# Optimization experiments

Measured on AMD Instinct MI355X. Metric: run time of the kernel, lower is better.

The kernel has to match this reference:

```python
import jax, jax.numpy as jnp
import numpy as np


def setup_inputs() -> dict:
    key = jax.random.key(0)
    ks = jax.random.split(key, 6)
    B, N, S, D, A = 32, 12, 512, 256, 96
    return {
        "value": jax.random.normal(ks[0], (B, N, S, D), dtype=jnp.float32),
        "emb": jax.random.normal(ks[1], (N, S, A), dtype=jnp.float32),
        "Wqk": jax.random.normal(ks[2], (A, D), dtype=jnp.float32) * (A ** -0.5),
        "bqk": jax.random.normal(ks[3], (D,), dtype=jnp.float32) * 0.02,
        "Wv": jax.random.normal(ks[4], (D, D), dtype=jnp.float32) * (D ** -0.5),
        "bv": jax.random.normal(ks[5], (D,), dtype=jnp.float32) * 0.02,
    }


def reference(value, emb, Wqk, bqk, Wv, bv):
    # qk: [n, s, d] -- query and key share the same projection FC_Q_K
    qk = emb @ Wqk + bqk
    v = value @ Wv + bv                      # [b, n, s, d]
    q = jax.nn.softmax(qk, axis=-1)          # softmax over d (last dim of query)
    k = jax.nn.softmax(qk.swapaxes(-1, -2), axis=-1)  # [n, d, s], softmax over s
    # key @ value: [n, d, s] x [b, n, s, e] -> [b, n, d, e] (broadcast over b)
    kv = jnp.einsum('nds,bnse->bnde', k, v)
    # query @ kv: [n, s, d] x [b, n, d, e] -> [b, n, s, e]
    out = jnp.einsum('nsd,bnde->bnse', q, kv)
    return out
```

## Files before the change

### kernel.cpp

```cpp
#include <hip/hip_runtime.h>
#include <hip/hip_bf16.h>

#define B_ 32
#define N_ 12
#define S_ 512
#define D_ 256
#define A_ 96

typedef __attribute__((ext_vector_type(8))) short short8;
typedef __attribute__((ext_vector_type(4))) float float4v;

static __device__ __forceinline__ ushort f2bf(float f) {
  union { float f; unsigned u; } a;
  a.f = f;
  return (ushort)((a.u + 0x7FFFu + ((a.u >> 16) & 1u)) >> 16);
}

__global__ __launch_bounds__(256) void k_qk_softmax_q(
    const float* __restrict__ emb, const float* __restrict__ Wqk,
    const float* __restrict__ bqk, float* __restrict__ qk,
    ushort* __restrict__ qb) {
  int ns = blockIdx.x;
  int d = threadIdx.x;
  __shared__ float se[A_];
  __shared__ float red[8];
  if (d < A_) se[d] = emb[ns * A_ + d];
  __syncthreads();
  float acc = bqk[d];
#pragma unroll
  for (int a = 0; a < A_; ++a) acc = fmaf(se[a], Wqk[a * D_ + d], acc);
  qk[ns * D_ + d] = acc;
  float m = acc;
  for (int off = 32; off; off >>= 1) m = fmaxf(m, __shfl_xor(m, off));
  if ((d & 63) == 0) red[d >> 6] = m;
  __syncthreads();
  m = fmaxf(fmaxf(red[0], red[1]), fmaxf(red[2], red[3]));
  float e = __expf(acc - m);
  float sum = e;
  for (int off = 32; off; off >>= 1) sum += __shfl_xor(sum, off);
  if ((d & 63) == 0) red[4 + (d >> 6)] = sum;
  __syncthreads();
  sum = red[4] + red[5] + red[6] + red[7];
  qb[ns * D_ + d] = f2bf(e / sum);
}

__global__ __launch_bounds__(256) void k_softmax_kT(
    const float* __restrict__ qk, ushort* __restrict__ kTb) {
  int d = blockIdx.x;
  int n = blockIdx.y;
  int s = threadIdx.x;
  __shared__ float red[8];
  float v0 = qk[(n * S_ + s) * D_ + d];
  float v1 = qk[(n * S_ + s + 256) * D_ + d];
  float m = fmaxf(v0, v1);
  for (int off = 32; off; off >>= 1) m = fmaxf(m, __shfl_xor(m, off));
  if ((s & 63) == 0) red[s >> 6] = m;
  __syncthreads();
  m = fmaxf(fmaxf(red[0], red[1]), fmaxf(red[2], red[3]));
  float e0 = __expf(v0 - m), e1 = __expf(v1 - m);
  float sum = e0 + e1;
  for (int off = 32; off; off >>= 1) sum += __shfl_xor(sum, off);
  if ((s & 63) == 0) red[4 + (s >> 6)] = sum;
  __syncthreads();
  sum = red[4] + red[5] + red[6] + red[7];
  float inv = 1.0f / sum;
  kTb[(n * D_ + d) * S_ + s] = f2bf(e0 * inv);
  kTb[(n * D_ + d) * S_ + s + 256] = f2bf(e1 * inv);
}

__global__ __launch_bounds__(256) void k_wvt(const float* __restrict__ Wv,
                                             ushort* __restrict__ WvT) {
  int c = blockIdx.x, e = threadIdx.x;
  WvT[c * D_ + e] = f2bf(Wv[e * D_ + c]);
}

__global__ __launch_bounds__(256) void k_kv0T(
    const ushort* __restrict__ kTb, const float* __restrict__ value,
    ushort* __restrict__ kv0T) {
  const int bx = blockIdx.x;
  const int by = blockIdx.y;
  const int bz = blockIdx.z;
  const int n = bz % N_;
  const int tid = threadIdx.x;
  const int l = tid & 63, w = tid >> 6;
  const int wm = w & 1, wn = w >> 1;
  const int lane16 = l & 15, quad = l >> 4;

  __shared__ ushort ldsA[128 * 72];
  __shared__ ushort ldsB[128 * 72];

  float4v acc[4][4];
#pragma unroll
  for (int i = 0; i < 4; ++i)
#pragma unroll
    for (int j = 0; j < 4; ++j) acc[i][j] = (float4v)0.0f;

  const ushort* kTbase = kTb + ((size_t)(n * D_ + bx * 128)) * S_;
  const float* vbase = value + (size_t)bz * S_ * D_ + by * 128;

  for (int sc = 0; sc < S_; sc += 64) {
    __syncthreads();
#pragma unroll
    for (int it = 0; it < 4; ++it) {
      int id = it * 256 + tid;
      int rd = id >> 3, cc = (id & 7) * 8;
      *(uint4*)(&ldsA[rd * 72 + cc]) =
          *(const uint4*)(kTbase + rd * S_ + sc + cc);
    }
#pragma unroll
    for (int it = 0; it < 16; ++it) {
      int id = it * 256 + tid;
      int e = id & 127, sp = id >> 7;
      float f0 = vbase[(sc + 2 * sp) * D_ + e];
      float f1 = vbase[(sc + 2 * sp + 1) * D_ + e];
      ushort2 p;
      p.x = f2bf(f0);
      p.y = f2bf(f1);
      *(ushort2*)(&ldsB[e * 72 + 2 * sp]) = p;
    }
    __syncthreads();
#pragma unroll
    for (int kc = 0; kc < 64; kc += 32) {
      int ko = kc + quad * 8;
      short8 a[4], b[4];
#pragma unroll
      for (int i = 0; i < 4; ++i)
        a[i] = *(const short8*)(&ldsA[(wm * 64 + i * 16 + lane16) * 72 + ko]);
#pragma unroll
      for (int j = 0; j < 4; ++j)
        b[j] = *(const short8*)(&ldsB[(wn * 64 + j * 16 + lane16) * 72 + ko]);
#pragma unroll
      for (int i = 0; i < 4; ++i)
#pragma unroll
        for (int j = 0; j < 4; ++j)
          acc[i][j] = __builtin_amdgcn_mfma_f32_16x16x32_bf16(a[i], b[j],
                                                              acc[i][j], 0, 0, 0);
    }
  }
  ushort* obase = kv0T + (size_t)bz * D_ * D_;
#pragma unroll
  for (int i = 0; i < 4; ++i) {
#pragma unroll
    for (int j = 0; j < 4; ++j) {
      int e = by * 128 + wn * 64 + j * 16 + lane16;
      int d0 = bx * 128 + wm * 64 + i * 16 + quad * 4;
      ushort4 p;
      p.x = f2bf(acc[i][j][0]);
      p.y = f2bf(acc[i][j][1]);
      p.z = f2bf(acc[i][j][2]);
      p.w = f2bf(acc[i][j][3]);
      *(ushort4*)(obase + e * D_ + d0) = p;
    }
  }
}

__global__ __launch_bounds__(256) void k_out_fused(
    const ushort* __restrict__ qb, const ushort* __restrict__ kv0T,
    const ushort* __restrict__ WvT, const float* __restrict__ bv,
    float* __restrict__ out) {
  const int bx = blockIdx.x;
  const int bz = blockIdx.y;
  const int n = bz % N_;
  const int tid = threadIdx.x;
  const int l = tid & 63, w = tid >> 6;
  const int lane16 = l & 15, quad = l >> 4;

  __shared__ ushort smem[35328];
  ushort* ldsKV = smem;
  ushort* ldsQ = smem + 18432;
  ushort* ldsW = smem;
  ushort* ldsT = smem + 18432;

  const ushort* qbase = qb + ((size_t)n * S_ + bx * 64) * D_;
  const ushort* kvbase = kv0T + (size_t)bz * D_ * D_;

  float4v acc[4][4];
#pragma unroll
  for (int i = 0; i < 4; ++i)
#pragma unroll
    for (int j = 0; j < 4; ++j) acc[i][j] = (float4v)0.0f;

  for (int dc = 0; dc < D_; dc += 64) {
    __syncthreads();
#pragma unroll
    for (int it = 0; it < 2; ++it) {
      int id = it * 256 + tid;
      int r = id >> 3, cc = (id & 7) * 8;
      *(uint4*)(&ldsQ[r * 72 + cc]) = *(const uint4*)(qbase + r * D_ + dc + cc);
    }
#pragma unroll
    for (int it = 0; it < 8; ++it) {
      int id = it * 256 + tid;
      int r = id >> 3, cc = (id & 7) * 8;
      *(uint4*)(&ldsKV[r * 72 + cc]) =
          *(const uint4*)(kvbase + r * D_ + dc + cc);
    }
    __syncthreads();
#pragma unroll
    for (int kc = 0; kc < 64; kc += 32) {
      int ko = kc + quad * 8;
      short8 a[4], b[4];
#pragma unroll
      for (int i = 0; i < 4; ++i)
        a[i] = *(const short8*)(&ldsKV[(w * 64 + i * 16 + lane16) * 72 + ko]);
#pragma unroll
      for (int j = 0; j < 4; ++j)
        b[j] = *(const short8*)(&ldsQ[(j * 16 + lane16) * 72 + ko]);
#pragma unroll
      for (int i = 0; i < 4; ++i)
#pragma unroll
        for (int j = 0; j < 4; ++j)
          acc[i][j] = __builtin_amdgcn_mfma_f32_16x16x32_bf16(a[i], b[j],
                                                              acc[i][j], 0, 0, 0);
    }
  }
  __syncthreads();
#pragma unroll
  for (int i = 0; i < 4; ++i) {
#pragma unroll
    for (int j = 0; j < 4; ++j) {
      int s = j * 16 + lane16;
      int e0 = w * 64 + i * 16 + quad * 4;
      ushort4 p;
      p.x = f2bf(acc[i][j][0]);
      p.y = f2bf(acc[i][j][1]);
      p.z = f2bf(acc[i][j][2]);
      p.w = f2bf(acc[i][j][3]);
      *(ushort4*)(&ldsT[s * 264 + e0]) = p;
    }
  }

  float4v acc2[4][4];
#pragma unroll
  for (int i = 0; i < 4; ++i)
#pragma unroll
    for (int j = 0; j < 4; ++j) acc2[i][j] = (float4v)0.0f;

  for (int ec = 0; ec < D_; ec += 64) {
    __syncthreads();
#pragma unroll
    for (int it = 0; it < 8; ++it) {
      int id = it * 256 + tid;
      int r = id >> 3, cc = (id & 7) * 8;
      *(uint4*)(&ldsW[r * 72 + cc]) = *(const uint4*)(WvT + r * D_ + ec + cc);
    }
    __syncthreads();
#pragma unroll
    for (int kc = 0; kc < 64; kc += 32) {
      int ko = kc + quad * 8;
      short8 a[4], b[4];
#pragma unroll
      for (int i = 0; i < 4; ++i)
        a[i] = *(const short8*)(&ldsT[(i * 16 + lane16) * 264 + ec + ko]);
#pragma unroll
      for (int j = 0; j < 4; ++j)
        b[j] = *(const short8*)(&ldsW[(w * 64 + j * 16 + lane16) * 72 + ko]);
#pragma unroll
      for (int i = 0; i < 4; ++i)
#pragma unroll
        for (int j = 0; j < 4; ++j)
          acc2[i][j] = __builtin_amdgcn_mfma_f32_16x16x32_bf16(a[i], b[j],
                                                               acc2[i][j], 0, 0, 0);
    }
  }
  float* obase = out + (size_t)bz * S_ * D_ + (size_t)bx * 64 * D_;
#pragma unroll
  for (int i = 0; i < 4; ++i) {
#pragma unroll
    for (int j = 0; j < 4; ++j) {
      int s0 = i * 16 + quad * 4;
      int c = w * 64 + j * 16 + lane16;
      float bvc = bv[c];
#pragma unroll
      for (int r = 0; r < 4; ++r)
        obase[(s0 + r) * D_ + c] = acc2[i][j][r] + bvc;
    }
  }
}

extern "C" void kernel_launch(void* const* d_in, const int* in_sizes, int n_in,
                              void* d_out, int out_size, void* d_ws,
                              size_t ws_size, hipStream_t stream) {
  const float* value = (const float*)d_in[0];
  const float* emb   = (const float*)d_in[1];
  const float* Wqk   = (const float*)d_in[2];
  const float* bqk   = (const float*)d_in[3];
  const float* Wv    = (const float*)d_in[4];
  const float* bv    = (const float*)d_in[5];
  float* out = (float*)d_out;

  char* ws = (char*)d_ws;
  float*  qk   = (float*)ws;
  ushort* qb   = (ushort*)(ws + 6291456);
  ushort* kTb  = (ushort*)(ws + 9437184);
  ushort* kv0T = (ushort*)(ws + 12582912);
  ushort* WvT  = (ushort*)(ws + 62914560);

  k_qk_softmax_q<<<dim3(N_ * S_), 256, 0, stream>>>(emb, Wqk, bqk, qk, qb);
  k_softmax_kT<<<dim3(D_, N_), 256, 0, stream>>>(qk, kTb);
  k_wvt<<<dim3(D_), 256, 0, stream>>>(Wv, WvT);
  k_kv0T<<<dim3(2, 2, B_ * N_), 256, 0, stream>>>(kTb, value, kv0T);
  k_out_fused<<<dim3(8, B_ * N_), 256, 0, stream>>>(qb, kv0T, WvT, bv, out);
}
```

Baseline: 483.7 us.

## Reassociate Wv into kv and split into three direct-to-LDS bf16 GEMMs

Adds a separate pass that transposes value and converts it to bf16. The per-(b,n) chain is then computed as three generic 128x128 GEMM kernels: kv0 = kT·v, then kv0 is multiplied by Wv (the reassociation, a 256x256x256 product), then q times that result plus bias. All three share a core that loads tiles with global_load_lds instead of register-staged copies. This removes the fused two-stage output kernel and its per-block Wv recompute, at the cost of an extra full transposed copy of value and more intermediate buffers written to and read from HBM. The unpadded 64-wide LDS rows may cause bank conflicts.

```diff
diff --git a/kernel.cpp b/kernel.cpp
--- a/kernel.cpp
+++ b/kernel.cpp
@@ -9,6 +9,13 @@
 
 typedef __attribute__((ext_vector_type(8))) short short8;
 typedef __attribute__((ext_vector_type(4))) float float4v;
+
+typedef const __attribute__((address_space(1))) void* gas_cvp;
+typedef __attribute__((address_space(3))) void* las_vp;
+
+static __device__ __forceinline__ void gl_lds16(const ushort* g, ushort* l) {
+  __builtin_amdgcn_global_load_lds((gas_cvp)g, (las_vp)l, 16, 0, 0);
+}
 
 static __device__ __forceinline__ ushort f2bf(float f) {
   union { float f; unsigned u; } a;
@@ -74,207 +81,152 @@
   WvT[c * D_ + e] = f2bf(Wv[e * D_ + c]);
 }
 
-__global__ __launch_bounds__(256) void k_kv0T(
-    const ushort* __restrict__ kTb, const float* __restrict__ value,
-    ushort* __restrict__ kv0T) {
-  const int bx = blockIdx.x;
-  const int by = blockIdx.y;
-  const int bz = blockIdx.z;
-  const int n = bz % N_;
+__global__ __launch_bounds__(256) void k_vT(const float* __restrict__ value,
+                                            ushort* __restrict__ vTb) {
+  const int s0 = blockIdx.x * 64;
+  const int e0 = blockIdx.y * 64;
+  const size_t bz = blockIdx.z;
+  __shared__ ushort lds[64 * 72];
+  const float* vb = value + bz * (size_t)(S_ * D_);
+  const int tid = threadIdx.x;
+#pragma unroll
+  for (int t = 0; t < 4; ++t) {
+    int id = t * 256 + tid;
+    int r = id >> 4;
+    int c4 = id & 15;
+    float4 f = *(const float4*)(vb + (size_t)(s0 + r) * D_ + e0 + c4 * 4);
+    lds[(c4 * 4 + 0) * 72 + r] = f2bf(f.x);
+    lds[(c4 * 4 + 1) * 72 + r] = f2bf(f.y);
+    lds[(c4 * 4 + 2) * 72 + r] = f2bf(f.z);
+    lds[(c4 * 4 + 3) * 72 + r] = f2bf(f.w);
+  }
+  __syncthreads();
+  ushort* ob = vTb + bz * (size_t)(D_ * S_);
+#pragma unroll
+  for (int t = 0; t < 2; ++t) {
+    int id = t * 256 + tid;
+    int e = id >> 3;
+    int c8 = id & 7;
+    *(uint4*)(ob + (size_t)(e0 + e) * S_ + s0 + c8 * 8) =
+        *(const uint4*)(&lds[e * 72 + c8 * 8]);
+  }
+}
+
+static __device__ __forceinline__ void gemm_core_128(
+    const ushort* __restrict__ A, const ushort* __restrict__ B, int lda,
+    int ldb, int K, ushort* ldsA, ushort* ldsB, float4v acc[4][4]) {
   const int tid = threadIdx.x;
   const int l = tid & 63, w = tid >> 6;
-  const int wm = w & 1, wn = w >> 1;
-  const int lane16 = l & 15, quad = l >> 4;
-
-  __shared__ ushort ldsA[128 * 72];
-  __shared__ ushort ldsB[128 * 72];
-
-  float4v acc[4][4];
+  const int lane16 = l & 15, quad = l >> 4;
+  const int wm = w & 1, wn = w >> 1;
+  const int lrow = l >> 3;
+  const int lcol = (l & 7) * 8;
 #pragma unroll
   for (int i = 0; i < 4; ++i)
 #pragma unroll
     for (int j = 0; j < 4; ++j) acc[i][j] = (float4v)0.0f;
-
-  const ushort* kTbase = kTb + ((size_t)(n * D_ + bx * 128)) * S_;
-  const float* vbase = value + (size_t)bz * S_ * D_ + by * 128;
-
-  for (int sc = 0; sc < S_; sc += 64) {
+  for (int kc = 0; kc < K; kc += 64) {
     __syncthreads();
 #pragma unroll
-    for (int it = 0; it < 4; ++it) {
-      int id = it * 256 + tid;
-      int rd = id >> 3, cc = (id & 7) * 8;
-      *(uint4*)(&ldsA[rd * 72 + cc]) =
-          *(const uint4*)(kTbase + rd * S_ + sc + cc);
-    }
-#pragma unroll
-    for (int it = 0; it < 16; ++it) {
-      int id = it * 256 + tid;
-      int e = id & 127, sp = id >> 7;
-      float f0 = vbase[(sc + 2 * sp) * D_ + e];
-      float f1 = vbase[(sc + 2 * sp + 1) * D_ + e];
-      ushort2 p;
-      p.x = f2bf(f0);
-      p.y = f2bf(f1);
-      *(ushort2*)(&ldsB[e * 72 + 2 * sp]) = p;
+    for (int t = 0; t < 4; ++t) {
+      int row = w * 32 + t * 8;
+      gl_lds16(A + (size_t)(row + lrow) * lda + kc + lcol,
+               &ldsA[row * 64]);
+      gl_lds16(B + (size_t)(row + lrow) * ldb + kc + lcol,
+               &ldsB[row * 64]);
     }
     __syncthreads();
 #pragma unroll
-    for (int kc = 0; kc < 64; kc += 32) {
-      int ko = kc + quad * 8;
+    for (int kk = 0; kk < 64; kk += 32) {
+      const int ko = kk + quad * 8;
       short8 a[4], b[4];
 #pragma unroll
       for (int i = 0; i < 4; ++i)
-        a[i] = *(const short8*)(&ldsA[(wm * 64 + i * 16 + lane16) * 72 + ko]);
+        a[i] = *(const short8*)&ldsA[(wm * 64 + i * 16 + lane16) * 64 + ko];
 #pragma unroll
       for (int j = 0; j < 4; ++j)
-        b[j] = *(const short8*)(&ldsB[(wn * 64 + j * 16 + lane16) * 72 + ko]);
+        b[j] = *(const short8*)&ldsB[(wn * 64 + j * 16 + lane16) * 64 + ko];
 #pragma unroll
       for (int i = 0; i < 4; ++i)
 #pragma unroll
         for (int j = 0; j < 4; ++j)
-          acc[i][j] = __builtin_amdgcn_mfma_f32_16x16x32_bf16(a[i], b[j],
-                                                              acc[i][j], 0, 0, 0);
+          acc[i][j] = __builtin_amdgcn_mfma_f32_16x16x32_bf16(
+              a[i], b[j], acc[i][j], 0, 0, 0);
     }
   }
-  ushort* obase = kv0T + (size_t)bz * D_ * D_;
-#pragma unroll
-  for (int i = 0; i < 4; ++i) {
-#pragma unroll
-    for (int j = 0; j < 4; ++j) {
-      int e = by * 128 + wn * 64 + j * 16 + lane16;
-      int d0 = bx * 128 + wm * 64 + i * 16 + quad * 4;
-      ushort4 p;
-      p.x = f2bf(acc[i][j][0]);
-      p.y = f2bf(acc[i][j][1]);
-      p.z = f2bf(acc[i][j][2]);
-      p.w = f2bf(acc[i][j][3]);
-      *(ushort4*)(obase + e * D_ + d0) = p;
-    }
-  }
-}
-
-__global__ __launch_bounds__(256) void k_out_fused(
-    const ushort* __restrict__ qb, const ushort* __restrict__ kv0T,
-    const ushort* __restrict__ WvT, const float* __restrict__ bv,
-    float* __restrict__ out) {
-  const int bx = blockIdx.x;
-  const int bz = blockIdx.y;
+}
+
+__global__ __launch_bounds__(256) void k_gemm1(
+    const ushort* __restrict__ kTb, const ushort* __restrict__ vTb,
+    ushort* __restrict__ kv0) {
+  __shared__ ushort ldsA[128 * 64], ldsB[128 * 64];
+  const int bx = blockIdx.x, by = blockIdx.y, bz = blockIdx.z;
   const int n = bz % N_;
-  const int tid = threadIdx.x;
-  const int l = tid & 63, w = tid >> 6;
-  const int lane16 = l & 15, quad = l >> 4;
-
-  __shared__ ushort smem[35328];
-  ushort* ldsKV = smem;
-  ushort* ldsQ = smem + 18432;
-  ushort* ldsW = smem;
-  ushort* ldsT = smem + 18432;
-
-  const ushort* qbase = qb + ((size_t)n * S_ + bx * 64) * D_;
-  const ushort* kvbase = kv0T + (size_t)bz * D_ * D_;
-
   float4v acc[4][4];
+  gemm_core_128(kTb + ((size_t)n * D_ + bx * 128) * S_,
+                vTb + ((size_t)bz * D_ + by * 128) * S_, S_, S_, S_, ldsA,
+                ldsB, acc);
+  const int l = threadIdx.x & 63, w = threadIdx.x >> 6;
+  const int lane16 = l & 15, quad = l >> 4;
+  const int wm = w & 1, wn = w >> 1;
+  ushort* C = kv0 + (size_t)bz * D_ * D_;
 #pragma unroll
   for (int i = 0; i < 4; ++i)
 #pragma unroll
-    for (int j = 0; j < 4; ++j) acc[i][j] = (float4v)0.0f;
-
-  for (int dc = 0; dc < D_; dc += 64) {
-    __syncthreads();
-#pragma unroll
-    for (int it = 0; it < 2; ++it) {
-      int id = it * 256 + tid;
-      int r = id >> 3, cc = (id & 7) * 8;
-      *(uint4*)(&ldsQ[r * 72 + cc]) = *(const uint4*)(qbase + r * D_ + dc + cc);
-    }
-#pragma unroll
-    for (int it = 0; it < 8; ++it) {
-      int id = it * 256 + tid;
-      int r = id >> 3, cc = (id & 7) * 8;
-      *(uint4*)(&ldsKV[r * 72 + cc]) =
-          *(const uint4*)(kvbase + r * D_ + dc + cc);
-    }
-    __syncthreads();
-#pragma unroll
-    for (int kc = 0; kc < 64; kc += 32) {
-      int ko = kc + quad * 8;
-      short8 a[4], b[4];
-#pragma unroll
-      for (int i = 0; i < 4; ++i)
-        a[i] = *(const short8*)(&ldsKV[(w * 64 + i * 16 + lane16) * 72 + ko]);
-#pragma unroll
-      for (int j = 0; j < 4; ++j)
-        b[j] = *(const short8*)(&ldsQ[(j * 16 + lane16) * 72 + ko]);
-#pragma unroll
-      for (int i = 0; i < 4; ++i)
-#pragma unroll
-        for (int j = 0; j < 4; ++j)
-          acc[i][j] = __builtin_amdgcn_mfma_f32_16x16x32_bf16(a[i], b[j],
-                                                              acc[i][j], 0, 0, 0);
-    }
-  }
-  __syncthreads();
-#pragma unroll
-  for (int i = 0; i < 4; ++i) {
-#pragma unroll
-    for (int j = 0; j < 4; ++j) {
-      int s = j * 16 + lane16;
-      int e0 = w * 64 + i * 16 + quad * 4;
-      ushort4 p;
-      p.x = f2bf(acc[i][j][0]);
-      p.y = f2bf(acc[i][j][1]);
-      p.z = f2bf(acc[i][j][2]);
-      p.w = f2bf(acc[i][j][3]);
-      *(ushort4*)(&ldsT[s * 264 + e0]) = p;
-    }
-  }
-
-  float4v acc2[4][4];
+    for (int j = 0; j < 4; ++j)
+#pragma unroll
+      for (int r = 0; r < 4; ++r)
+        C[(size_t)(bx * 128 + wm * 64 + i * 16 + quad * 4 + r) * D_ +
+          by * 128 + wn * 64 + j * 16 + lane16] = f2bf(acc[i][j][r]);
+}
+
+__global__ __launch_bounds__(256) void k_gemm2(
+    const ushort* __restrict__ WvT, const ushort* __restrict__ kv0,
+    ushort* __restrict__ kvWT) {
+  __shared__ ushort ldsA[128 * 64], ldsB[128 * 64];
+  const int bx = blockIdx.x, by = blockIdx.y, bz = blockIdx.z;
+  float4v acc[4][4];
+  gemm_core_128(WvT + (size_t)(bx * 128) * D_,
+                kv0 + (size_t)bz * D_ * D_ + (size_t)(by * 128) * D_, D_, D_,
+                D_, ldsA, ldsB, acc);
+  const int l = threadIdx.x & 63, w = threadIdx.x >> 6;
+  const int lane16 = l & 15, quad = l >> 4;
+  const int wm = w & 1, wn = w >> 1;
+  ushort* C = kvWT + (size_t)bz * D_ * D_;
 #pragma unroll
   for (int i = 0; i < 4; ++i)
 #pragma unroll
-    for (int j = 0; j < 4; ++j) acc2[i][j] = (float4v)0.0f;
-
-  for (int ec = 0; ec < D_; ec += 64) {
-    __syncthreads();
-#pragma unroll
-    for (int it = 0; it < 8; ++it) {
-      int id = it * 256 + tid;
-      int r = id >> 3, cc = (id & 7) * 8;
-      *(uint4*)(&ldsW[r * 72 + cc]) = *(const uint4*)(WvT + r * D_ + ec + cc);
-    }
-    __syncthreads();
-#pragma unroll
-    for (int kc = 0; kc < 64; kc += 32) {
-      int ko = kc + quad * 8;
-      short8 a[4], b[4];
-#pragma unroll
-      for (int i = 0; i < 4; ++i)
-        a[i] = *(const short8*)(&ldsT[(i * 16 + lane16) * 264 + ec + ko]);
-#pragma unroll
-      for (int j = 0; j < 4; ++j)
-        b[j] = *(const short8*)(&ldsW[(w * 64 + j * 16 + lane16) * 72 + ko]);
-#pragma unroll
-      for (int i = 0; i < 4; ++i)
-#pragma unroll
-        for (int j = 0; j < 4; ++j)
-          acc2[i][j] = __builtin_amdgcn_mfma_f32_16x16x32_bf16(a[i], b[j],
-                                                               acc2[i][j], 0, 0, 0);
-    }
-  }
-  float* obase = out + (size_t)bz * S_ * D_ + (size_t)bx * 64 * D_;
-#pragma unroll
-  for (int i = 0; i < 4; ++i) {
-#pragma unroll
-    for (int j = 0; j < 4; ++j) {
-      int s0 = i * 16 + quad * 4;
-      int c = w * 64 + j * 16 + lane16;
-      float bvc = bv[c];
+    for (int j = 0; j < 4; ++j)
 #pragma unroll
       for (int r = 0; r < 4; ++r)
-        obase[(s0 + r) * D_ + c] = acc2[i][j][r] + bvc;
-    }
+        C[(size_t)(bx * 128 + wm * 64 + i * 16 + quad * 4 + r) * D_ +
+          by * 128 + wn * 64 + j * 16 + lane16] = f2bf(acc[i][j][r]);
+}
+
+__global__ __launch_bounds__(256) void k_gemm3(
+    const ushort* __restrict__ qb, const ushort* __restrict__ kvWT,
+    const float* __restrict__ bv, float* __restrict__ out) {
+  __shared__ ushort ldsA[128 * 64], ldsB[128 * 64];
+  const int bx = blockIdx.x, by = blockIdx.y, bz = blockIdx.z;
+  const int n = bz % N_;
+  float4v acc[4][4];
+  gemm_core_128(qb + ((size_t)n * S_ + bx * 128) * D_,
+                kvWT + (size_t)bz * D_ * D_ + (size_t)(by * 128) * D_, D_, D_,
+                D_, ldsA, ldsB, acc);
+  const int l = threadIdx.x & 63, w = threadIdx.x >> 6;
+  const int lane16 = l & 15, quad = l >> 4;
+  const int wm = w & 1, wn = w >> 1;
+  float* C = out + (size_t)bz * S_ * D_;
+#pragma unroll
+  for (int j = 0; j < 4; ++j) {
+    const int c = by * 128 + wn * 64 + j * 16 + lane16;
+    const float bvc = bv[c];
+#pragma unroll
+    for (int i = 0; i < 4; ++i)
+#pragma unroll
+      for (int r = 0; r < 4; ++r)
+        C[(size_t)(bx * 128 + wm * 64 + i * 16 + quad * 4 + r) * D_ + c] =
+            acc[i][j][r] + bvc;
   }
 }
 
@@ -293,12 +245,16 @@
   float*  qk   = (float*)ws;
   ushort* qb   = (ushort*)(ws + 6291456);
   ushort* kTb  = (ushort*)(ws + 9437184);
-  ushort* kv0T = (ushort*)(ws + 12582912);
-  ushort* WvT  = (ushort*)(ws + 62914560);
+  ushort* WvT  = (ushort*)(ws + 12582912);
+  ushort* vTb  = (ushort*)(ws + 12713984);
+  ushort* kv0  = (ushort*)(ws + 113377280);
+  ushort* kvWT = (ushort*)(ws + 163708928);
 
   k_qk_softmax_q<<<dim3(N_ * S_), 256, 0, stream>>>(emb, Wqk, bqk, qk, qb);
   k_softmax_kT<<<dim3(D_, N_), 256, 0, stream>>>(qk, kTb);
   k_wvt<<<dim3(D_), 256, 0, stream>>>(Wv, WvT);
-  k_kv0T<<<dim3(2, 2, B_ * N_), 256, 0, stream>>>(kTb, value, kv0T);
-  k_out_fused<<<dim3(8, B_ * N_), 256, 0, stream>>>(qb, kv0T, WvT, bv, out);
-}
+  k_vT<<<dim3(8, 4, B_ * N_), 256, 0, stream>>>(value, vTb);
+  k_gemm1<<<dim3(2, 2, B_ * N_), 256, 0, stream>>>(kTb, vTb, kv0);
+  k_gemm2<<<dim3(2, 2, B_ * N_), 256, 0, stream>>>(WvT, kv0, kvWT);
+  k_gemm3<<<dim3(4, 2, B_ * N_), 256, 0, stream>>>(qb, kvWT, bv, out);
+}
```

Result: slower. 524.0 us (+8.3%).
